# Optimization experiments

Hardware: AMD Instinct MI355X
Metric: run time of the kernel (lower is better)

Reference implementation:

```python
import jax, jax.numpy as jnp
import numpy as np

B, D0, D1, D2 = 512, 4096, 4096, 4096
W_SCALE = 0.01  # small init so sigmoids stay in a useful range


def setup_inputs() -> dict:
    key = jax.random.key(0)
    k0, k1, k2, k3, k4 = jax.random.split(key, 5)
    return {
        "data": jax.random.uniform(k0, (B, D0), dtype=jnp.float32),
        "W1": jax.random.normal(k1, (D0, D1), dtype=jnp.float32) * W_SCALE,
        "W2": jax.random.normal(k2, (D1, D2), dtype=jnp.float32) * W_SCALE,
        "b1": jax.random.normal(k3, (D1,), dtype=jnp.float32),
        "b2": jax.random.normal(k4, (D2,), dtype=jnp.float32),
        "iterations": 10,
    }


def reference(data, W1, W2, b1, b2, iterations):
    """Mean-field conditional sample of a 3-layer DBM (visible clamped to data).

    Faithful to conditional_sample_general_meanfield with mean_cond (sigmoid
    of bias + interaction), sample_state[0]=False, invtemperature=1.0.
    Schedule per iteration: odd layers (j=1) then even layers (j=2).
    """
    beta = jnp.float32(1.0)
    nb = data.shape[0]
    # initial states: layer mean activations broadcast over the batch
    s1 = jnp.broadcast_to(jax.nn.sigmoid(b1), (nb, b1.shape[0]))
    s2 = jnp.broadcast_to(jax.nn.sigmoid(b2), (nb, b2.shape[0]))

    def gibbs_step(carry, _):
        s1, s2 = carry
        # j=1: interaction from below (gradOutput: data @ W1) and above (gradInput: s2 @ W2^T)
        s1 = jax.nn.sigmoid(b1 + beta * (data @ W1 + s2 @ W2.T))
        # j=2: interaction from below (gradOutput: s1 @ W2); j=0 clamped
        s2 = jax.nn.sigmoid(b2 + beta * (s1 @ W2))
        return (s1, s2), None

    (s1, s2), _ = jax.lax.scan(gibbs_step, (s1, s2), None, length=iterations)
    # original returns [state0, state1, state2]; state0 == data (clamped)
    return jnp.stack([s1, s2])  # [2, B, D]
```

## Files before the change

kernel.cpp:

```cpp
#include <hip/hip_runtime.h>


typedef __bf16 bf16_t;
typedef __attribute__((ext_vector_type(8))) __bf16 bf16x8;
typedef __attribute__((ext_vector_type(4))) __bf16 bf16x4;
typedef __attribute__((ext_vector_type(4))) float f32x4;
typedef __attribute__((ext_vector_type(2))) _Float16 half2v;
typedef __attribute__((ext_vector_type(8))) _Float16 f16x8;

typedef const __attribute__((address_space(1))) void* gptr_t;
typedef __attribute__((address_space(3))) void* lptr_t;

constexpr int M = 512, N = 4096, K = 4096;
constexpr int BM = 256, BN = 256, BK = 64;
constexpr int SPLIT = 8;
constexpr int KSLICE = K / SPLIT;
constexpr int PHASES = KSLICE / BK;
constexpr int NTILES = (M / BM) * (N / BN);
constexpr int TILE_H2 = BM * BN / 2;


__global__ __launch_bounds__(256) void prep_w(const float* __restrict__ in,
                                              bf16_t* __restrict__ outT,
                                              bf16_t* __restrict__ outC) {
  __shared__ float t[64][65];
  const int tid = threadIdx.x;
  const int x0 = blockIdx.x * 64, y0 = blockIdx.y * 64;
  const int row = tid >> 4;
  const int xs  = tid & 15;
#pragma unroll
  for (int i = 0; i < 4; ++i) {
    const int r = row + 16 * i;
    float4 v = *(const float4*)(in + (size_t)(y0 + r) * 4096 + x0 + xs * 4);
    t[xs * 4 + 0][r] = v.x;
    t[xs * 4 + 1][r] = v.y;
    t[xs * 4 + 2][r] = v.z;
    t[xs * 4 + 3][r] = v.w;
  }
  __syncthreads();
#pragma unroll
  for (int j = 0; j < 2; ++j) {
    const int idx = tid + 256 * j;
    const int xr = idx >> 3, sg = idx & 7;
    bf16x8 v;
#pragma unroll
    for (int e = 0; e < 8; ++e) v[e] = (bf16_t)t[xr][sg * 8 + e];
    *(bf16x8*)(outT + (size_t)(x0 + xr) * 4096 + y0 + sg * 8) = v;
  }
  if (outC) {
#pragma unroll
    for (int j = 0; j < 2; ++j) {
      const int idx = tid + 256 * j;
      const int yr = idx >> 3, sg = idx & 7;
      bf16x8 v;
#pragma unroll
      for (int e = 0; e < 8; ++e) v[e] = (bf16_t)t[sg * 8 + e][yr];
      *(bf16x8*)(outC + (size_t)(y0 + yr) * 4096 + x0 + sg * 8) = v;
    }
  }
}

__global__ __launch_bounds__(256) void cvt_bf16(const float* __restrict__ in,
                                                bf16_t* __restrict__ out) {
  const size_t i8 = ((size_t)blockIdx.x * 256 + threadIdx.x) * 8;
  float4 a = *(const float4*)(in + i8);
  float4 b = *(const float4*)(in + i8 + 4);
  bf16x8 o;
  o[0] = (bf16_t)a.x; o[1] = (bf16_t)a.y; o[2] = (bf16_t)a.z; o[3] = (bf16_t)a.w;
  o[4] = (bf16_t)b.x; o[5] = (bf16_t)b.y; o[6] = (bf16_t)b.z; o[7] = (bf16_t)b.w;
  *(bf16x8*)(out + i8) = o;
}

__global__ __launch_bounds__(256) void init_s2(const float* __restrict__ b2,
                                               bf16_t* __restrict__ s2, int total) {
  int i = blockIdx.x * 256 + threadIdx.x;
  if (i < total) {
    float x = b2[i & (N - 1)];
    s2[i] = (bf16_t)(1.0f / (1.0f + __expf(-x)));
  }
}

__global__ __launch_bounds__(512, 2) void gemm_bt(
    const bf16_t* __restrict__ A,
    const bf16_t* __restrict__ BT,
    _Float16* __restrict__ slabs) {
  __shared__ __align__(16) bf16_t sA[2 * BM * BK];
  __shared__ __align__(16) bf16_t sB[2 * BN * BK];

  const int gid = blockIdx.x;
  const int z = gid & 7;
  const int rem = gid >> 3;
  const int tx = rem & 15;
  const int ty = rem >> 4;
  const int tile = ty * 16 + tx;

  const int tid = threadIdx.x;
  const int wid = tid >> 6;
  const int l   = tid & 63;
  const int r   = l & 15;
  const int q   = l >> 4;
  const int wm  = wid & 1;
  const int wn  = wid >> 1;

  const bf16_t* Ab = A + (size_t)(ty * BM) * K + (size_t)z * KSLICE;
  const bf16_t* Bb = BT + (size_t)(tx * BN) * K + (size_t)z * KSLICE;

  const int srow8 = l >> 3;
  const int scol  = ((l & 7) ^ srow8) * 8;

  f32x4 acc[8][4];
  const f32x4 zero = {0.0f, 0.0f, 0.0f, 0.0f};
#pragma unroll
  for (int i = 0; i < 8; ++i)
#pragma unroll
    for (int j = 0; j < 4; ++j) acc[i][j] = zero;

  auto issue = [&](int ph, int pb) {
    const size_t kof = (size_t)ph * BK;
#pragma unroll
    for (int i = 0; i < 4; ++i) {
      const int rg = wid * 4 + i;
      const int row = rg * 8 + srow8;
      __builtin_amdgcn_global_load_lds(
          (gptr_t)(Ab + (size_t)row * K + kof + scol),
          (lptr_t)(sA + pb * (BM * BK) + rg * 512), 16, 0, 0);
      __builtin_amdgcn_global_load_lds(
          (gptr_t)(Bb + (size_t)row * K + kof + scol),
          (lptr_t)(sB + pb * (BN * BK) + rg * 512), 16, 0, 0);
    }
  };

  issue(0, 0);
  for (int ph = 0; ph < PHASES; ++ph) {
    const int pb = ph & 1;
    __syncthreads();
    if (ph + 1 < PHASES) issue(ph + 1, pb ^ 1);

    const bf16_t* sAp = sA + pb * (BM * BK);
    const bf16_t* sBp = sB + pb * (BN * BK);
#pragma unroll
    for (int kk = 0; kk < 2; ++kk) {
      bf16x8 af[8], bfr[4];
#pragma unroll
      for (int mt = 0; mt < 8; ++mt) {
        const int rowm = wm * 128 + mt * 16 + r;
        const int sl = (kk * 4 + q) ^ (r & 7);
        af[mt] = *(const bf16x8*)(sAp + rowm * BK + sl * 8);
      }
#pragma unroll
      for (int nt = 0; nt < 4; ++nt) {
        const int rown = wn * 64 + nt * 16 + r;
        const int sl = (kk * 4 + q) ^ (r & 7);
        bfr[nt] = *(const bf16x8*)(sBp + rown * BK + sl * 8);
      }
#pragma unroll
      for (int mt = 0; mt < 8; ++mt)
#pragma unroll
        for (int nt = 0; nt < 4; ++nt)
          acc[mt][nt] = __builtin_amdgcn_mfma_f32_16x16x32_bf16(
              af[mt], bfr[nt], acc[mt][nt], 0, 0, 0);
    }
  }

  half2v* P2 = (half2v*)slabs + ((size_t)z * NTILES + tile) * TILE_H2;
#pragma unroll
  for (int mt = 0; mt < 8; ++mt)
#pragma unroll
    for (int nt = 0; nt < 4; ++nt)
#pragma unroll
      for (int i2 = 0; i2 < 2; ++i2) {
        half2v h;
        h[0] = (_Float16)acc[mt][nt][2 * i2];
        h[1] = (_Float16)acc[mt][nt][2 * i2 + 1];
        __builtin_nontemporal_store(
            h, P2 + (size_t)((((wid * 8 + mt) * 4 + nt) * 2 + i2) * 64 + l));
      }
}

template <int MODE>
__global__ __launch_bounds__(256) void epi(const _Float16* __restrict__ slabs,
                                           const float* __restrict__ bias,
                                           const bf16_t* __restrict__ C0b,
                                           bf16_t* __restrict__ outb,
                                           float* __restrict__ outf) {
  const int g = blockIdx.x * 256 + threadIdx.x;
  const int tile = g >> 13;
  const int gi = g & 8191;
  const int slot = gi >> 4;
  const int l4 = (gi & 15) * 4;

  float s0[4] = {0.f, 0.f, 0.f, 0.f};
  float s1[4] = {0.f, 0.f, 0.f, 0.f};
  const size_t ubase = (size_t)tile * TILE_H2 + slot * 64 + l4;
#pragma unroll
  for (int zz = 0; zz < SPLIT; ++zz) {
    f16x8 v = *(const f16x8*)((const half2v*)slabs +
                              (size_t)zz * NTILES * TILE_H2 + ubase);
#pragma unroll
    for (int j = 0; j < 4; ++j) {
      s0[j] += (float)v[2 * j];
      s1[j] += (float)v[2 * j + 1];
    }
  }

  const int i2 = slot & 1, nt = (slot >> 1) & 3, mt = (slot >> 3) & 7,
            wid = slot >> 6;
  const int wm = wid & 1, wn = wid >> 1;
  const int q = (gi & 15) >> 2, rb = (gi & 3) * 4;
  const int ty = tile >> 4, tx = tile & 15;
  const int row = ty * 256 + wm * 128 + mt * 16 + q * 4 + 2 * i2;
  const int col = tx * 256 + wn * 64 + nt * 16 + rb;
  const size_t i0 = (size_t)row * N + col;
  const size_t i1 = i0 + N;

  if (MODE == 0) {
    bf16x4 o0, o1;
#pragma unroll
    for (int j = 0; j < 4; ++j) { o0[j] = (bf16_t)s0[j]; o1[j] = (bf16_t)s1[j]; }
    *(bf16x4*)(outb + i0) = o0;
    *(bf16x4*)(outb + i1) = o1;
    return;
  }
  const float4 bv = *(const float4*)(bias + col);
  s0[0] += bv.x; s0[1] += bv.y; s0[2] += bv.z; s0[3] += bv.w;
  s1[0] += bv.x; s1[1] += bv.y; s1[2] += bv.z; s1[3] += bv.w;
  if (MODE == 1) {
    bf16x4 c0 = *(const bf16x4*)(C0b + i0);
    bf16x4 c1 = *(const bf16x4*)(C0b + i1);
#pragma unroll
    for (int j = 0; j < 4; ++j) { s0[j] += (float)c0[j]; s1[j] += (float)c1[j]; }
  }
  float v0[4], v1[4];
  bf16x4 o0, o1;
#pragma unroll
  for (int j = 0; j < 4; ++j) {
    v0[j] = 1.0f / (1.0f + __expf(-s0[j]));
    v1[j] = 1.0f / (1.0f + __expf(-s1[j]));
    o0[j] = (bf16_t)v0[j];
    o1[j] = (bf16_t)v1[j];
  }
  *(bf16x4*)(outb + i0) = o0;
  *(bf16x4*)(outb + i1) = o1;
  if (outf) {
    float4 f0 = {v0[0], v0[1], v0[2], v0[3]};
    float4 f1 = {v1[0], v1[1], v1[2], v1[3]};
    *(float4*)(outf + i0) = f0;
    *(float4*)(outf + i1) = f1;
  }
}


extern "C" void kernel_launch(void* const* d_in, const int* in_sizes, int n_in,
                              void* d_out, int out_size, void* d_ws, size_t ws_size,
                              hipStream_t stream) {
  const float* data = (const float*)d_in[0];
  const float* W1   = (const float*)d_in[1];
  const float* W2   = (const float*)d_in[2];
  const float* b1   = (const float*)d_in[3];
  const float* b2   = (const float*)d_in[4];

  char* p = (char*)d_ws;
  bf16_t* W1T = (bf16_t*)p; p += (size_t)K * N * 2;
  bf16_t* W2b = (bf16_t*)p; p += (size_t)K * N * 2;
  bf16_t* W2T = (bf16_t*)p; p += (size_t)K * N * 2;
  bf16_t* C0b = (bf16_t*)p; p += (size_t)M * N * 2;
  bf16_t* s1b = (bf16_t*)p; p += (size_t)M * N * 2;
  bf16_t* s2b = (bf16_t*)p; p += (size_t)M * N * 2;
  bf16_t* dat = (bf16_t*)p; p += (size_t)M * K * 2;

  _Float16* slabC = (_Float16*)W2T;
  _Float16* slab  = (_Float16*)W1T;

  float* out_s1 = (float*)d_out;
  float* out_s2 = out_s1 + (size_t)M * N;

  cvt_bf16<<<(M * K) / 2048, 256, 0, stream>>>(data, dat);
  prep_w<<<dim3(64, 64), 256, 0, stream>>>(W1, W1T, (bf16_t*)nullptr);

  const int gblocks = NTILES * SPLIT;
  const int epiblocks = (M * N / 8) / 256;

  gemm_bt<<<gblocks, 512, 0, stream>>>(dat, W1T, slabC);
  epi<0><<<epiblocks, 256, 0, stream>>>(slabC, nullptr, nullptr, C0b, nullptr);

  prep_w<<<dim3(64, 64), 256, 0, stream>>>(W2, W2T, W2b);
  init_s2<<<(M * N) / 256, 256, 0, stream>>>(b2, s2b, M * N);

  for (int it = 0; it < 10; ++it) {
    const bool last = (it == 9);
    gemm_bt<<<gblocks, 512, 0, stream>>>(s2b, W2b, slab);
    epi<1><<<epiblocks, 256, 0, stream>>>(slab, b1, C0b, s1b,
                                          last ? out_s1 : (float*)nullptr);
    gemm_bt<<<gblocks, 512, 0, stream>>>(s1b, W2T, slab);
    epi<2><<<epiblocks, 256, 0, stream>>>(slab, b2, nullptr, s2b,
                                          last ? out_s2 : (float*)nullptr);
  }
}
```

Baseline: 802.6 us.

## Split GEMM K-tiles into half-planes with finer-grained staged prefetch and MFMA priority

Restructures the bf16 GEMM main loop so each 64-wide K tile is stored as two 32-wide LDS planes per matrix and buffer. The next tile's half-planes are prefetched between fragment reads, with explicit vmcnt waits and raw barriers instead of __syncthreads. MFMA clusters are wrapped in s_setprio so compute gets priority over memory traffic. The goal is better overlap of global-to-LDS loads with matrix math, at the cost of more barriers and removing the XOR swizzle, which may bring back LDS bank conflicts.

```diff
diff --git a/kernel.cpp b/kernel.cpp
--- a/kernel.cpp
+++ b/kernel.cpp
@@ -15,9 +15,10 @@
 constexpr int BM = 256, BN = 256, BK = 64;
 constexpr int SPLIT = 8;
 constexpr int KSLICE = K / SPLIT;
-constexpr int PHASES = KSLICE / BK;
+constexpr int KTILES = KSLICE / BK;
 constexpr int NTILES = (M / BM) * (N / BN);
 constexpr int TILE_H2 = BM * BN / 2;
+constexpr int PLANE = 256 * 32;
 
 
 __global__ __launch_bounds__(256) void prep_w(const float* __restrict__ in,
@@ -84,8 +85,7 @@
     const bf16_t* __restrict__ A,
     const bf16_t* __restrict__ BT,
     _Float16* __restrict__ slabs) {
-  __shared__ __align__(16) bf16_t sA[2 * BM * BK];
-  __shared__ __align__(16) bf16_t sB[2 * BN * BK];
+  __shared__ __align__(16) bf16_t lds[8 * PLANE];
 
   const int gid = blockIdx.x;
   const int z = gid & 7;
@@ -105,8 +105,33 @@
   const bf16_t* Ab = A + (size_t)(ty * BM) * K + (size_t)z * KSLICE;
   const bf16_t* Bb = BT + (size_t)(tx * BN) * K + (size_t)z * KSLICE;
 
-  const int srow8 = l >> 3;
-  const int scol  = ((l & 7) ^ srow8) * 8;
+  const int srow = l >> 2;
+  const int scol = (l & 3) * 8;
+
+  auto plane = [&](int b, int mat, int kk) -> bf16_t* {
+    return lds + ((size_t)((b * 2 + mat) * 2 + kk)) * PLANE;
+  };
+
+  auto stage = [&](int tt, int kk) {
+    const int b = tt & 1;
+    const size_t kof = (size_t)tt * BK + kk * 32;
+#pragma unroll
+    for (int i = 0; i < 2; ++i) {
+      const int ch = wid * 2 + i;
+      const int row = ch * 16 + srow;
+      __builtin_amdgcn_global_load_lds(
+          (gptr_t)(Ab + (size_t)row * K + kof + scol),
+          (lptr_t)(plane(b, 0, kk) + ch * 512), 16, 0, 0);
+    }
+#pragma unroll
+    for (int i = 0; i < 2; ++i) {
+      const int ch = wid * 2 + i;
+      const int row = ch * 16 + srow;
+      __builtin_amdgcn_global_load_lds(
+          (gptr_t)(Bb + (size_t)row * K + kof + scol),
+          (lptr_t)(plane(b, 1, kk) + ch * 512), 16, 0, 0);
+    }
+  };
 
   f32x4 acc[8][4];
   const f32x4 zero = {0.0f, 0.0f, 0.0f, 0.0f};
@@ -115,52 +140,73 @@
 #pragma unroll
     for (int j = 0; j < 4; ++j) acc[i][j] = zero;
 
-  auto issue = [&](int ph, int pb) {
-    const size_t kof = (size_t)ph * BK;
-#pragma unroll
-    for (int i = 0; i < 4; ++i) {
-      const int rg = wid * 4 + i;
-      const int row = rg * 8 + srow8;
-      __builtin_amdgcn_global_load_lds(
-          (gptr_t)(Ab + (size_t)row * K + kof + scol),
-          (lptr_t)(sA + pb * (BM * BK) + rg * 512), 16, 0, 0);
-      __builtin_amdgcn_global_load_lds(
-          (gptr_t)(Bb + (size_t)row * K + kof + scol),
-          (lptr_t)(sB + pb * (BN * BK) + rg * 512), 16, 0, 0);
-    }
-  };
-
-  issue(0, 0);
-  for (int ph = 0; ph < PHASES; ++ph) {
-    const int pb = ph & 1;
-    __syncthreads();
-    if (ph + 1 < PHASES) issue(ph + 1, pb ^ 1);
-
-    const bf16_t* sAp = sA + pb * (BM * BK);
-    const bf16_t* sBp = sB + pb * (BN * BK);
-#pragma unroll
-    for (int kk = 0; kk < 2; ++kk) {
-      bf16x8 af[8], bfr[4];
-#pragma unroll
-      for (int mt = 0; mt < 8; ++mt) {
-        const int rowm = wm * 128 + mt * 16 + r;
-        const int sl = (kk * 4 + q) ^ (r & 7);
-        af[mt] = *(const bf16x8*)(sAp + rowm * BK + sl * 8);
-      }
-#pragma unroll
-      for (int nt = 0; nt < 4; ++nt) {
-        const int rown = wn * 64 + nt * 16 + r;
-        const int sl = (kk * 4 + q) ^ (r & 7);
-        bfr[nt] = *(const bf16x8*)(sBp + rown * BK + sl * 8);
-      }
-#pragma unroll
-      for (int mt = 0; mt < 8; ++mt)
-#pragma unroll
-        for (int nt = 0; nt < 4; ++nt)
-          acc[mt][nt] = __builtin_amdgcn_mfma_f32_16x16x32_bf16(
-              af[mt], bfr[nt], acc[mt][nt], 0, 0, 0);
-    }
-  }
+#define MMA_CLUSTER(AF, MB)                                                  \
+  __builtin_amdgcn_s_setprio(1);                                             \
+  _Pragma("unroll") for (int mt = 0; mt < 4; ++mt)                           \
+      _Pragma("unroll") for (int nt = 0; nt < 4; ++nt)                       \
+          acc[(MB) + mt][nt] = __builtin_amdgcn_mfma_f32_16x16x32_bf16(      \
+              AF[mt], bfr[nt], acc[(MB) + mt][nt], 0, 0, 0);                 \
+  __builtin_amdgcn_s_setprio(0);
+
+  stage(0, 0);
+  stage(0, 1);
+  asm volatile("s_waitcnt vmcnt(4)" ::: "memory");
+  __builtin_amdgcn_s_barrier();
+  __builtin_amdgcn_sched_barrier(0);
+
+  for (int t = 0; t < KTILES; ++t) {
+    const int b = t & 1;
+    const bf16_t* pA0 = plane(b, 0, 0);
+    const bf16_t* pA1 = plane(b, 0, 1);
+    const bf16_t* pB0 = plane(b, 1, 0);
+    const bf16_t* pB1 = plane(b, 1, 1);
+    const int arow0 = (wm * 128 + r) * 32 + q * 8;
+    const int brow  = (wn * 64 + r) * 32 + q * 8;
+
+    {
+      bf16x8 bfr[4], af0[4], af1[4];
+#pragma unroll
+      for (int nt = 0; nt < 4; ++nt)
+        bfr[nt] = *(const bf16x8*)(pB0 + brow + nt * (16 * 32));
+#pragma unroll
+      for (int mt = 0; mt < 4; ++mt)
+        af0[mt] = *(const bf16x8*)(pA0 + arow0 + mt * (16 * 32));
+      if (t + 1 < KTILES) stage(t + 1, 0);
+      MMA_CLUSTER(af0, 0)
+#pragma unroll
+      for (int mt = 0; mt < 4; ++mt)
+        af1[mt] = *(const bf16x8*)(pA0 + arow0 + (64 * 32) + mt * (16 * 32));
+      MMA_CLUSTER(af1, 4)
+    }
+    if (t + 1 < KTILES)
+      asm volatile("s_waitcnt vmcnt(4)" ::: "memory");
+    else
+      asm volatile("s_waitcnt vmcnt(0)" ::: "memory");
+    __builtin_amdgcn_s_barrier();
+    __builtin_amdgcn_sched_barrier(0);
+
+    {
+      bf16x8 bfr[4], af0[4], af1[4];
+#pragma unroll
+      for (int nt = 0; nt < 4; ++nt)
+        bfr[nt] = *(const bf16x8*)(pB1 + brow + nt * (16 * 32));
+#pragma unroll
+      for (int mt = 0; mt < 4; ++mt)
+        af0[mt] = *(const bf16x8*)(pA1 + arow0 + mt * (16 * 32));
+      if (t + 1 < KTILES) stage(t + 1, 1);
+      MMA_CLUSTER(af0, 0)
+#pragma unroll
+      for (int mt = 0; mt < 4; ++mt)
+        af1[mt] = *(const bf16x8*)(pA1 + arow0 + (64 * 32) + mt * (16 * 32));
+      MMA_CLUSTER(af1, 4)
+    }
+    if (t + 1 < KTILES) {
+      asm volatile("s_waitcnt vmcnt(4)" ::: "memory");
+      __builtin_amdgcn_s_barrier();
+      __builtin_amdgcn_sched_barrier(0);
+    }
+  }
+#undef MMA_CLUSTER
 
   half2v* P2 = (half2v*)slabs + ((size_t)z * NTILES + tile) * TILE_H2;
 #pragma unroll
```

Measured after the change: 773.8 us. 3.6% less time.
